# Performance work log

Measured on AMD Instinct MI355X. Metric: run time of the kernel, lower is better.

Reference implementation:

```python
import jax, jax.numpy as jnp
import numpy as np

NUM_NODES = 50000
NUM_EDGES = 1600000
NUM_GRAPHS = 64
K_HOPS = 3


def setup_inputs() -> dict:
    key = jax.random.key(0)
    ks = jax.random.split(key, 8)
    d_in, d_h, d_out = 128, 512, 16
    x = jax.random.normal(ks[0], (NUM_NODES, d_in), dtype=jnp.float32)
    edge_index = jax.random.randint(ks[1], (2, NUM_EDGES), 0, NUM_NODES, dtype=jnp.int64)
    batch = jnp.sort(jax.random.randint(ks[2], (NUM_NODES,), 0, NUM_GRAPHS, dtype=jnp.int64))
    w1 = jax.random.normal(ks[3], (d_in, d_h), dtype=jnp.float32) / np.sqrt(d_in)
    b1 = jnp.zeros((d_h,), dtype=jnp.float32)
    w2 = jax.random.normal(ks[4], (d_h, d_h), dtype=jnp.float32) / np.sqrt(d_h)
    b2 = jnp.zeros((d_h,), dtype=jnp.float32)
    wc = jax.random.normal(ks[5], (d_h, d_out), dtype=jnp.float32) / np.sqrt(d_h)
    bc = jnp.zeros((d_out,), dtype=jnp.float32)
    return {"x": x, "edge_index": edge_index, "batch": batch,
            "w1": w1, "b1": b1, "w2": w2, "b2": b2, "wc": wc, "bc": bc}


def _propagate(x, row, col, norm):
    # one hop: out[r] += x[c] * norm  (degree-normalized scatter-add)
    msg = x[col] * norm[:, None]                      # [E+N, d]
    return jax.ops.segment_sum(msg, row, num_segments=NUM_NODES)


def reference(x, edge_index, batch, w1, b1, w2, b2, wc, bc):
    # add self loops
    loops = jnp.arange(NUM_NODES, dtype=edge_index.dtype)
    row = jnp.concatenate([edge_index[0], loops])
    col = jnp.concatenate([edge_index[1], loops])
    deg = jax.ops.segment_sum(jnp.ones_like(row, dtype=jnp.float32), row,
                              num_segments=NUM_NODES)
    deg = jnp.clip(deg, 1.0)
    norm = 1.0 / deg[row]                             # [E+N]
    # K-hop propagation (eval mode: dropout / drop_node inactive)
    h = x
    for _ in range(K_HOPS):
        h = _propagate(h, row, col, norm)
    # MLP
    h = jax.nn.relu(h @ w1 + b1)
    h = h @ w2 + b2
    # global mean pool over graphs
    sums = jax.ops.segment_sum(h, batch, num_segments=NUM_GRAPHS)
    cnts = jax.ops.segment_sum(jnp.ones((h.shape[0],), dtype=h.dtype), batch,
                               num_segments=NUM_GRAPHS)
    pooled = sums / jnp.clip(cnts, 1.0)[:, None]      # [G, d_h]
    return pooled @ wc + bc                            # [G, out]
```

## Files before the change

kernel.cpp:

```cpp
#include <hip/hip_runtime.h>
#include <hip/hip_bf16.h>
#include <hip/hip_fp8.h>

#define N_NODES 50000
#define N_EDGES 1600000
#define N_GRAPHS 64
#define D_IN 128
#define D_H 512
#define D_OUT 16

#define NBUK 196
#define BUK_CAP 9216
#define P1_EDGES 8192
#define P1_BLOCKS ((N_EDGES + P1_EDGES - 1) / P1_EDGES)

typedef short bf16x8 __attribute__((ext_vector_type(8)));
typedef float f32x4 __attribute__((ext_vector_type(4)));

static __device__ __forceinline__ unsigned short f2bf(float f) {
    __hip_bfloat16 h = __float2bfloat16(f);
    return *(unsigned short*)&h;
}

static __device__ __forceinline__ float2 fp8x2_dec(unsigned short u) {
    __hip_fp8x2_e4m3 p;
    p.__x = (__hip_fp8x2_storage_t)u;
    return static_cast<float2>(p);
}

static __device__ __forceinline__ unsigned short fp8x2_enc(float a, float b) {
    __hip_fp8_e4m3 pa(a), pb(b);
    return (unsigned short)((unsigned)pa.__x | ((unsigned)pb.__x << 8));
}


__global__ __launch_bounds__(256) void partition_edges(const int* __restrict__ row,
                                                       const int* __restrict__ col,
                                                       int* __restrict__ bucket_cnt,
                                                       unsigned* __restrict__ edge_buf) {
    __shared__ unsigned recs[P1_EDGES];
    __shared__ unsigned sorted[P1_EDGES];
    __shared__ int hist4[4][NBUK];
    __shared__ int cur4[4][NBUK];
    __shared__ int gbase[NBUK];
    __shared__ int scan[256];
    int tid = threadIdx.x;
    int wave = tid >> 6;
    int e0 = blockIdx.x * P1_EDGES;
    int m = N_EDGES - e0; if (m > P1_EDGES) m = P1_EDGES;

    for (int i = tid; i < 4 * NBUK; i += 256) ((int*)hist4)[i] = 0;
    for (int i = tid; i < 4 * NBUK; i += 256) ((int*)cur4)[i] = 0;
    __syncthreads();
    for (int i = tid; i < m; i += 256) {
        int r = row[e0 + i];
        int c = col[e0 + i];
        int buk = r >> 8;
        recs[i] = ((unsigned)buk << 24) | ((unsigned)(r & 255) << 16) | (unsigned)c;
        atomicAdd(&hist4[wave][buk], 1);
    }
    __syncthreads();
    int tot = 0;
    if (tid < NBUK) tot = hist4[0][tid] + hist4[1][tid] + hist4[2][tid] + hist4[3][tid];
    scan[tid] = (tid < NBUK) ? tot : 0;
    __syncthreads();
    for (int off = 1; off < 256; off <<= 1) {
        int v = (tid >= off) ? scan[tid - off] : 0;
        __syncthreads();
        scan[tid] += v;
        __syncthreads();
    }
    if (tid < NBUK) {
        int run = (tid == 0) ? 0 : scan[tid - 1];
        gbase[tid] = (tot > 0) ? atomicAdd(&bucket_cnt[tid], tot) : 0;
#pragma unroll
        for (int w = 0; w < 4; ++w) {
            int c = hist4[w][tid];
            hist4[w][tid] = run;
            run += c;
        }
    }
    __syncthreads();
    for (int i = tid; i < m; i += 256) {
        unsigned rec = recs[i];
        int buk = rec >> 24;
        int rank = atomicAdd(&cur4[wave][buk], 1);
        sorted[hist4[wave][buk] + rank] = rec;
    }
    __syncthreads();
    for (int p = tid; p < m; p += 256) {
        unsigned rec = sorted[p];
        int buk = rec >> 24;
        edge_buf[(size_t)buk * BUK_CAP + gbase[buk] + (p - hist4[0][buk])] = rec;
    }
}

__global__ __launch_bounds__(256) void finalize_csr(const unsigned* __restrict__ edge_buf,
                                                    const int* __restrict__ bucket_cnt,
                                                    int* __restrict__ rowptr,
                                                    float* __restrict__ invdeg,
                                                    unsigned short* __restrict__ csr_col) {
    __shared__ int hist[256], excl[256], cur[256], scan[256];
    int b = blockIdx.x;
    int tid = threadIdx.x;
    scan[tid] = (tid < NBUK) ? bucket_cnt[tid] : 0;
    __syncthreads();
    for (int off = 1; off < 256; off <<= 1) {
        int v = (tid >= off) ? scan[tid - off] : 0;
        __syncthreads();
        scan[tid] += v;
        __syncthreads();
    }
    int cnt = bucket_cnt[b];
    int base = (b == 0) ? 0 : scan[b - 1];
    const unsigned* src = edge_buf + (size_t)b * BUK_CAP;
    __syncthreads();
    hist[tid] = 0; cur[tid] = 0;
    __syncthreads();
    for (int i = tid; i < cnt; i += 256)
        atomicAdd(&hist[(src[i] >> 16) & 255], 1);
    __syncthreads();
    scan[tid] = hist[tid];
    __syncthreads();
    for (int off = 1; off < 256; off <<= 1) {
        int v = (tid >= off) ? scan[tid - off] : 0;
        __syncthreads();
        scan[tid] += v;
        __syncthreads();
    }
    excl[tid] = (tid == 0) ? 0 : scan[tid - 1];
    __syncthreads();
    int r = b * 256 + tid;
    if (r < N_NODES) {
        rowptr[r] = base + excl[tid];
        invdeg[r] = 1.0f / (float)(hist[tid] + 1);
    }
    if (b == NBUK - 1 && tid == 0) rowptr[N_NODES] = base + cnt;
    for (int i = tid; i < cnt; i += 256) {
        unsigned rec = src[i];
        int rl = (rec >> 16) & 255;
        int pos = excl[rl] + atomicAdd(&cur[rl], 1);
        csr_col[base + pos] = (unsigned short)(rec & 0xFFFFu);
    }
}


__global__ __launch_bounds__(256) void convert_x(const float* __restrict__ x,
                                                 unsigned short* __restrict__ xf, int npairs) {
    int i = blockIdx.x * 256 + threadIdx.x;
    if (i < npairs) {
        float2 v = ((const float2*)x)[i];
        xf[i] = fp8x2_enc(v.x, v.y);
    }
}

__global__ __launch_bounds__(256) void make_w1p(const float* __restrict__ w1,
                                                unsigned short* __restrict__ w1p) {
    int i = blockIdx.x * 256 + threadIdx.x;
    int j = i & 7, lane = (i >> 3) & 63, s = (i >> 9) & 3, t = i >> 11;
    int k = s * 32 + (lane >> 4) * 8 + j;
    int n = t * 16 + (lane & 15);
    w1p[i] = f2bf(w1[(size_t)k * D_H + n]);
}

__global__ __launch_bounds__(256) void fold_w(const float* __restrict__ w2,
                                              const float* __restrict__ wc,
                                              const float* __restrict__ b2,
                                              const float* __restrict__ bc,
                                              const int* __restrict__ batch,
                                              float* __restrict__ wcomb,
                                              float* __restrict__ bcomb,
                                              int* __restrict__ gcnt) {
    int tid = threadIdx.x;
    if (blockIdx.x == 33) {
        if (tid < N_GRAPHS) {
            int g = tid;
            int lo = 0, hi = N_NODES;
            while (lo < hi) { int mid = (lo + hi) >> 1; if (batch[mid] < g) lo = mid + 1; else hi = mid; }
            int a = lo;
            lo = 0; hi = N_NODES;
            while (lo < hi) { int mid = (lo + hi) >> 1; if (batch[mid] < g + 1) lo = mid + 1; else hi = mid; }
            gcnt[g] = lo - a;
        }
        return;
    }
    int o = tid & 15, kl = tid >> 4;
    int k = blockIdx.x * 16 + kl;
    if (k > D_H) return;
    const float* wr = (k < D_H) ? (w2 + (size_t)k * D_H) : b2;
    float s = 0.f;
    for (int j = 0; j < D_H; j += 4) {
        s += wr[j + 0] * wc[(j + 0) * D_OUT + o]
           + wr[j + 1] * wc[(j + 1) * D_OUT + o]
           + wr[j + 2] * wc[(j + 2) * D_OUT + o]
           + wr[j + 3] * wc[(j + 3) * D_OUT + o];
    }
    if (k < D_H) wcomb[k * D_OUT + o] = s;
    else         bcomb[o] = s + bc[o];
}


__global__ __launch_bounds__(128) void propagate_fp8(const unsigned short* __restrict__ xin,
                                                     unsigned short* __restrict__ out8,
                                                     unsigned* __restrict__ out16,
                                                     int last, float extra,
                                                     const int* __restrict__ rowptr,
                                                     const unsigned short* __restrict__ csr_col,
                                                     const float* __restrict__ invdeg) {
    int wave = threadIdx.x >> 6;
    int lane = threadIdx.x & 63;
    int r = blockIdx.x * 2 + wave;
    if (r >= N_NODES) return;
    int beg = rowptr[r], end = rowptr[r + 1];
    float2 sv = fp8x2_dec(xin[(size_t)r * 64 + lane]);
    float acc0 = sv.x, acc1 = sv.y;
    for (int cs = beg; cs < end; cs += 64) {
        int nn = end - cs; if (nn > 64) nn = 64;
        int colv = (int)csr_col[cs + (lane < nn ? lane : 0)];
        int j = 0;
        for (; j + 16 <= nn; j += 16) {
            unsigned short uu[16];
#pragma unroll
            for (int q = 0; q < 16; ++q) {
                int c = __shfl(colv, j + q, 64);
                uu[q] = xin[(size_t)c * 64 + lane];
            }
#pragma unroll
            for (int q = 0; q < 16; ++q) {
                float2 v = fp8x2_dec(uu[q]);
                acc0 += v.x; acc1 += v.y;
            }
        }
        for (; j + 4 <= nn; j += 4) {
            unsigned short u0, u1, u2, u3;
            {
                int c0 = __shfl(colv, j + 0, 64), c1 = __shfl(colv, j + 1, 64);
                int c2 = __shfl(colv, j + 2, 64), c3 = __shfl(colv, j + 3, 64);
                u0 = xin[(size_t)c0 * 64 + lane];
                u1 = xin[(size_t)c1 * 64 + lane];
                u2 = xin[(size_t)c2 * 64 + lane];
                u3 = xin[(size_t)c3 * 64 + lane];
            }
            float2 v0 = fp8x2_dec(u0), v1 = fp8x2_dec(u1);
            float2 v2 = fp8x2_dec(u2), v3 = fp8x2_dec(u3);
            acc0 += v0.x + v1.x + v2.x + v3.x;
            acc1 += v0.y + v1.y + v2.y + v3.y;
        }
        for (; j < nn; ++j) {
            int c = __shfl(colv, j, 64);
            float2 v = fp8x2_dec(xin[(size_t)c * 64 + lane]);
            acc0 += v.x; acc1 += v.y;
        }
    }
    float s = invdeg[r] * extra;
    acc0 *= s; acc1 *= s;
    if (last) {
        out16[(size_t)r * 64 + lane] = (unsigned)f2bf(acc0) | ((unsigned)f2bf(acc1) << 16);
    } else {
        out8[(size_t)r * 64 + lane] = fp8x2_enc(acc0, acc1);
    }
}


__global__ __launch_bounds__(256) void gemm_mfma_pool(const unsigned short* __restrict__ h3b,
                                                      const unsigned short* __restrict__ w1p,
                                                      const float* __restrict__ b1,
                                                      const int* __restrict__ batch,
                                                      float* __restrict__ gsum) {
    __shared__ float hls[64][132];
    __shared__ int bls[64];
    int tid = threadIdx.x;
    int lane = tid & 63, wave = tid >> 6;
    int quad = lane >> 4, l15 = lane & 15;
    int mbase = blockIdx.x * 64;
    int nbase = blockIdx.y * 128;

    int m = mbase + wave * 16 + l15;
    int mc = m < N_NODES ? m : N_NODES - 1;
    const unsigned short* arow = h3b + (size_t)mc * 128 + quad * 8;
    bf16x8 afrag[4];
#pragma unroll
    for (int s = 0; s < 4; ++s)
        afrag[s] = *(const bf16x8*)(arow + s * 32);

    f32x4 acc[8];
#pragma unroll
    for (int t = 0; t < 8; ++t) acc[t] = (f32x4){0.f, 0.f, 0.f, 0.f};

    const unsigned short* bbase = w1p + ((size_t)(blockIdx.y * 8) * 4 * 64 + lane) * 8;
#pragma unroll
    for (int t = 0; t < 8; ++t) {
#pragma unroll
        for (int s = 0; s < 4; ++s) {
            bf16x8 bfrag = *(const bf16x8*)(bbase + (size_t)(t * 4 + s) * 64 * 8);
            acc[t] = __builtin_amdgcn_mfma_f32_16x16x32_bf16(afrag[s], bfrag, acc[t], 0, 0, 0);
        }
    }

    if (tid < 64) {
        int mm = mbase + tid;
        bls[tid] = (mm < N_NODES) ? batch[mm] : 0;
    }
#pragma unroll
    for (int t = 0; t < 8; ++t)
#pragma unroll
        for (int rg = 0; rg < 4; ++rg)
            hls[wave * 16 + quad * 4 + rg][t * 16 + l15] = acc[t][rg];
    __syncthreads();

    int c = tid & 127, half = tid >> 7;
    float bias = b1[nbase + c];
    int r0 = half * 32;
    int cur = bls[r0];
    float s = 0.f;
    for (int r = r0; r < r0 + 32; ++r) {
        int mm = mbase + r;
        if (mm >= N_NODES) break;
        int g = bls[r];
        float v = hls[r][c] + bias;
        v = v > 0.f ? v : 0.f;
        if (g != cur) { atomicAdd(&gsum[cur * D_H + nbase + c], s); s = 0.f; cur = g; }
        s += v;
    }
    atomicAdd(&gsum[cur * D_H + nbase + c], s);
}


__global__ __launch_bounds__(256) void final_pool(const float* __restrict__ gsum,
                                                  const int* __restrict__ gcnt,
                                                  const float* __restrict__ wcomb,
                                                  const float* __restrict__ bcomb,
                                                  float* __restrict__ out) {
    int g = blockIdx.x;
    int tid = threadIdx.x;
    __shared__ float p[D_H];
    __shared__ float part[16][17];
    int c = gcnt[g]; if (c < 1) c = 1;
    float inv = 1.0f / (float)c;
    p[tid] = gsum[g * D_H + tid] * inv;
    p[tid + 256] = gsum[g * D_H + tid + 256] * inv;
    __syncthreads();
    int o = tid & 15, ch = tid >> 4;
    int k0 = ch * 32;
    float s = 0.f;
    for (int k = k0; k < k0 + 32; ++k)
        s += p[k] * wcomb[k * D_OUT + o];
    part[ch][o] = s;
    __syncthreads();
    if (tid < D_OUT) {
        float t = bcomb[tid];
        for (int ch2 = 0; ch2 < 16; ++ch2) t += part[ch2][tid];
        out[g * D_OUT + tid] = t;
    }
}


extern "C" void kernel_launch(void* const* d_in, const int* in_sizes, int n_in,
                              void* d_out, int out_size, void* d_ws, size_t ws_size,
                              hipStream_t stream) {
    const float* x     = (const float*)d_in[0];
    const int*   eidx  = (const int*)d_in[1];
    const int*   batch = (const int*)d_in[2];
    const float* w1    = (const float*)d_in[3];
    const float* b1    = (const float*)d_in[4];
    const float* w2    = (const float*)d_in[5];
    const float* b2    = (const float*)d_in[6];
    const float* wc    = (const float*)d_in[7];
    const float* bc    = (const float*)d_in[8];
    float* out = (float*)d_out;
    const int* row = eidx;
    const int* col = eidx + N_EDGES;

    char* p = (char*)d_ws;
    auto alloc = [&](size_t bytes) { char* q = p; p += (bytes + 255) & ~(size_t)255; return q; };
    char* zbase = p;
    int*   bucket_cnt = (int*)alloc((size_t)NBUK * 4);
    float* gsum       = (float*)alloc((size_t)N_GRAPHS * D_H * 4);
    size_t zbytes = (size_t)(p - zbase);
    int*   rowptr  = (int*)alloc((size_t)(N_NODES + 1) * 4);
    int*   gcnt    = (int*)alloc((size_t)N_GRAPHS * 4);
    float* invdeg  = (float*)alloc((size_t)N_NODES * 4);
    float* wcomb   = (float*)alloc((size_t)D_H * D_OUT * 4);
    float* bcomb   = (float*)alloc((size_t)D_OUT * 4);
    unsigned* edge_buf = (unsigned*)alloc((size_t)NBUK * BUK_CAP * 4);
    unsigned short* csr_col = (unsigned short*)alloc((size_t)N_EDGES * 2);
    unsigned short* xf  = (unsigned short*)alloc((size_t)N_NODES * 64 * 2);
    unsigned short* h0f = (unsigned short*)alloc((size_t)N_NODES * 64 * 2);
    unsigned short* h1f = (unsigned short*)alloc((size_t)N_NODES * 64 * 2);
    unsigned* h3b  = (unsigned*)alloc((size_t)N_NODES * 64 * 4);
    unsigned short* w1p = (unsigned short*)alloc((size_t)D_IN * D_H * 2);

    (void)hipMemsetAsync(zbase, 0, zbytes, stream);

    convert_x<<<(N_NODES * 64 + 255) / 256, 256, 0, stream>>>(x, xf, N_NODES * 64);
    make_w1p<<<(D_IN * D_H) / 256, 256, 0, stream>>>(w1, w1p);
    fold_w<<<34, 256, 0, stream>>>(w2, wc, b2, bc, batch, wcomb, bcomb, gcnt);

    partition_edges<<<P1_BLOCKS, 256, 0, stream>>>(row, col, bucket_cnt, edge_buf);
    finalize_csr<<<NBUK, 256, 0, stream>>>(edge_buf, bucket_cnt, rowptr, invdeg, csr_col);

    int pgrid = (N_NODES + 1) / 2;
    propagate_fp8<<<pgrid, 128, 0, stream>>>(xf,  h0f, nullptr, 0, 8.0f,
                                             rowptr, csr_col, invdeg);
    propagate_fp8<<<pgrid, 128, 0, stream>>>(h0f, h1f, nullptr, 0, 8.0f,
                                             rowptr, csr_col, invdeg);
    propagate_fp8<<<pgrid, 128, 0, stream>>>(h1f, nullptr, h3b, 1, 1.0f / 64.0f,
                                             rowptr, csr_col, invdeg);

    dim3 ggrid((N_NODES + 63) / 64, D_H / 128);
    gemm_mfma_pool<<<ggrid, 256, 0, stream>>>((const unsigned short*)h3b, w1p, b1, batch, gsum);
    final_pool<<<N_GRAPHS, 256, 0, stream>>>(gsum, gcnt, wcomb, bcomb, out);
}
```

Baseline: 287.9 us.

## Use finer CSR buckets with larger blocks and fuse prep kernels

Halves the row-bucket width from 256 to 128 rows, which doubles the bucket count and halves the per-block edge chunk, and runs partition and finalize with 512 threads. The goal is more CSR-build parallelism: more finalize blocks and less shared memory per partition block. Separately, the x-to-fp8 conversion, the w1 repack and the weight folding are merged into one launch to cut launch overhead. The trade-off is longer scans and more global bucket atomics per block, and the buffer capacity of 4608 leaves less slack for skewed buckets.

```diff
diff --git a/kernel.cpp b/kernel.cpp
--- a/kernel.cpp
+++ b/kernel.cpp
@@ -9,9 +9,9 @@
 #define D_H 512
 #define D_OUT 16
 
-#define NBUK 196
-#define BUK_CAP 9216
-#define P1_EDGES 8192
+#define NBUK 391
+#define BUK_CAP 4608
+#define P1_EDGES 4096
 #define P1_BLOCKS ((N_EDGES + P1_EDGES - 1) / P1_EDGES)
 
 typedef short bf16x8 __attribute__((ext_vector_type(8)));
@@ -34,7 +34,7 @@
 }
 
 
-__global__ __launch_bounds__(256) void partition_edges(const int* __restrict__ row,
+__global__ __launch_bounds__(512) void partition_edges(const int* __restrict__ row,
                                                        const int* __restrict__ col,
                                                        int* __restrict__ bucket_cnt,
                                                        unsigned* __restrict__ edge_buf) {
@@ -43,28 +43,28 @@
     __shared__ int hist4[4][NBUK];
     __shared__ int cur4[4][NBUK];
     __shared__ int gbase[NBUK];
-    __shared__ int scan[256];
+    __shared__ int scan[512];
     int tid = threadIdx.x;
-    int wave = tid >> 6;
+    int w2 = tid >> 7;
     int e0 = blockIdx.x * P1_EDGES;
     int m = N_EDGES - e0; if (m > P1_EDGES) m = P1_EDGES;
 
-    for (int i = tid; i < 4 * NBUK; i += 256) ((int*)hist4)[i] = 0;
-    for (int i = tid; i < 4 * NBUK; i += 256) ((int*)cur4)[i] = 0;
-    __syncthreads();
-    for (int i = tid; i < m; i += 256) {
+    for (int i = tid; i < 4 * NBUK; i += 512) ((int*)hist4)[i] = 0;
+    for (int i = tid; i < 4 * NBUK; i += 512) ((int*)cur4)[i] = 0;
+    __syncthreads();
+    for (int i = tid; i < m; i += 512) {
         int r = row[e0 + i];
         int c = col[e0 + i];
-        int buk = r >> 8;
-        recs[i] = ((unsigned)buk << 24) | ((unsigned)(r & 255) << 16) | (unsigned)c;
-        atomicAdd(&hist4[wave][buk], 1);
+        int buk = r >> 7;
+        recs[i] = ((unsigned)buk << 23) | ((unsigned)(r & 127) << 16) | (unsigned)c;
+        atomicAdd(&hist4[w2][buk], 1);
     }
     __syncthreads();
     int tot = 0;
     if (tid < NBUK) tot = hist4[0][tid] + hist4[1][tid] + hist4[2][tid] + hist4[3][tid];
     scan[tid] = (tid < NBUK) ? tot : 0;
     __syncthreads();
-    for (int off = 1; off < 256; off <<= 1) {
+    for (int off = 1; off < 512; off <<= 1) {
         int v = (tid >= off) ? scan[tid - off] : 0;
         __syncthreads();
         scan[tid] += v;
@@ -81,31 +81,32 @@
         }
     }
     __syncthreads();
-    for (int i = tid; i < m; i += 256) {
+    for (int i = tid; i < m; i += 512) {
         unsigned rec = recs[i];
-        int buk = rec >> 24;
-        int rank = atomicAdd(&cur4[wave][buk], 1);
-        sorted[hist4[wave][buk] + rank] = rec;
-    }
-    __syncthreads();
-    for (int p = tid; p < m; p += 256) {
+        int buk = rec >> 23;
+        int rank = atomicAdd(&cur4[w2][buk], 1);
+        sorted[hist4[w2][buk] + rank] = rec;
+    }
+    __syncthreads();
+    for (int p = tid; p < m; p += 512) {
         unsigned rec = sorted[p];
-        int buk = rec >> 24;
+        int buk = rec >> 23;
         edge_buf[(size_t)buk * BUK_CAP + gbase[buk] + (p - hist4[0][buk])] = rec;
     }
 }
 
-__global__ __launch_bounds__(256) void finalize_csr(const unsigned* __restrict__ edge_buf,
+__global__ __launch_bounds__(512) void finalize_csr(const unsigned* __restrict__ edge_buf,
                                                     const int* __restrict__ bucket_cnt,
                                                     int* __restrict__ rowptr,
                                                     float* __restrict__ invdeg,
                                                     unsigned short* __restrict__ csr_col) {
-    __shared__ int hist[256], excl[256], cur[256], scan[256];
+    __shared__ int hist[128], excl[128], cur[128];
+    __shared__ int scan[512];
     int b = blockIdx.x;
     int tid = threadIdx.x;
     scan[tid] = (tid < NBUK) ? bucket_cnt[tid] : 0;
     __syncthreads();
-    for (int off = 1; off < 256; off <<= 1) {
+    for (int off = 1; off < 512; off <<= 1) {
         int v = (tid >= off) ? scan[tid - off] : 0;
         __syncthreads();
         scan[tid] += v;
@@ -115,64 +116,66 @@
     int base = (b == 0) ? 0 : scan[b - 1];
     const unsigned* src = edge_buf + (size_t)b * BUK_CAP;
     __syncthreads();
-    hist[tid] = 0; cur[tid] = 0;
-    __syncthreads();
-    for (int i = tid; i < cnt; i += 256)
-        atomicAdd(&hist[(src[i] >> 16) & 255], 1);
-    __syncthreads();
-    scan[tid] = hist[tid];
-    __syncthreads();
-    for (int off = 1; off < 256; off <<= 1) {
+    if (tid < 128) { hist[tid] = 0; cur[tid] = 0; }
+    __syncthreads();
+    for (int i = tid; i < cnt; i += 512)
+        atomicAdd(&hist[(src[i] >> 16) & 127], 1);
+    __syncthreads();
+    scan[tid] = (tid < 128) ? hist[tid] : 0;
+    __syncthreads();
+    for (int off = 1; off < 512; off <<= 1) {
         int v = (tid >= off) ? scan[tid - off] : 0;
         __syncthreads();
         scan[tid] += v;
         __syncthreads();
     }
-    excl[tid] = (tid == 0) ? 0 : scan[tid - 1];
-    __syncthreads();
-    int r = b * 256 + tid;
-    if (r < N_NODES) {
+    if (tid < 128) excl[tid] = (tid == 0) ? 0 : scan[tid - 1];
+    __syncthreads();
+    int r = b * 128 + tid;
+    if (tid < 128 && r < N_NODES) {
         rowptr[r] = base + excl[tid];
         invdeg[r] = 1.0f / (float)(hist[tid] + 1);
     }
     if (b == NBUK - 1 && tid == 0) rowptr[N_NODES] = base + cnt;
-    for (int i = tid; i < cnt; i += 256) {
+    for (int i = tid; i < cnt; i += 512) {
         unsigned rec = src[i];
-        int rl = (rec >> 16) & 255;
+        int rl = (rec >> 16) & 127;
         int pos = excl[rl] + atomicAdd(&cur[rl], 1);
         csr_col[base + pos] = (unsigned short)(rec & 0xFFFFu);
     }
 }
 
 
-__global__ __launch_bounds__(256) void convert_x(const float* __restrict__ x,
-                                                 unsigned short* __restrict__ xf, int npairs) {
-    int i = blockIdx.x * 256 + threadIdx.x;
-    if (i < npairs) {
+__global__ __launch_bounds__(256) void prep(const float* __restrict__ x,
+                                            unsigned short* __restrict__ xf,
+                                            const float* __restrict__ w1,
+                                            unsigned short* __restrict__ w1p,
+                                            const float* __restrict__ w2,
+                                            const float* __restrict__ wc,
+                                            const float* __restrict__ b2,
+                                            const float* __restrict__ bc,
+                                            const int* __restrict__ batch,
+                                            float* __restrict__ wcomb,
+                                            float* __restrict__ bcomb,
+                                            int* __restrict__ gcnt) {
+    int b = blockIdx.x;
+    int tid = threadIdx.x;
+    if (b < 12500) {
+        int i = b * 256 + tid;
         float2 v = ((const float2*)x)[i];
         xf[i] = fp8x2_enc(v.x, v.y);
-    }
-}
-
-__global__ __launch_bounds__(256) void make_w1p(const float* __restrict__ w1,
-                                                unsigned short* __restrict__ w1p) {
-    int i = blockIdx.x * 256 + threadIdx.x;
-    int j = i & 7, lane = (i >> 3) & 63, s = (i >> 9) & 3, t = i >> 11;
-    int k = s * 32 + (lane >> 4) * 8 + j;
-    int n = t * 16 + (lane & 15);
-    w1p[i] = f2bf(w1[(size_t)k * D_H + n]);
-}
-
-__global__ __launch_bounds__(256) void fold_w(const float* __restrict__ w2,
-                                              const float* __restrict__ wc,
-                                              const float* __restrict__ b2,
-                                              const float* __restrict__ bc,
-                                              const int* __restrict__ batch,
-                                              float* __restrict__ wcomb,
-                                              float* __restrict__ bcomb,
-                                              int* __restrict__ gcnt) {
-    int tid = threadIdx.x;
-    if (blockIdx.x == 33) {
+        return;
+    }
+    if (b < 12756) {
+        int i = (b - 12500) * 256 + tid;
+        int j = i & 7, lane = (i >> 3) & 63, s = (i >> 9) & 3, t = i >> 11;
+        int k = s * 32 + (lane >> 4) * 8 + j;
+        int n = t * 16 + (lane & 15);
+        w1p[i] = f2bf(w1[(size_t)k * D_H + n]);
+        return;
+    }
+    int fb = b - 12756;
+    if (fb == 33) {
         if (tid < N_GRAPHS) {
             int g = tid;
             int lo = 0, hi = N_NODES;
@@ -185,7 +188,7 @@
         return;
     }
     int o = tid & 15, kl = tid >> 4;
-    int k = blockIdx.x * 16 + kl;
+    int k = fb * 16 + kl;
     if (k > D_H) return;
     const float* wr = (k < D_H) ? (w2 + (size_t)k * D_H) : b2;
     float s = 0.f;
@@ -392,12 +395,11 @@
 
     (void)hipMemsetAsync(zbase, 0, zbytes, stream);
 
-    convert_x<<<(N_NODES * 64 + 255) / 256, 256, 0, stream>>>(x, xf, N_NODES * 64);
-    make_w1p<<<(D_IN * D_H) / 256, 256, 0, stream>>>(w1, w1p);
-    fold_w<<<34, 256, 0, stream>>>(w2, wc, b2, bc, batch, wcomb, bcomb, gcnt);
-
-    partition_edges<<<P1_BLOCKS, 256, 0, stream>>>(row, col, bucket_cnt, edge_buf);
-    finalize_csr<<<NBUK, 256, 0, stream>>>(edge_buf, bucket_cnt, rowptr, invdeg, csr_col);
+    prep<<<12790, 256, 0, stream>>>(x, xf, w1, w1p, w2, wc, b2, bc, batch,
+                                    wcomb, bcomb, gcnt);
+
+    partition_edges<<<P1_BLOCKS, 512, 0, stream>>>(row, col, bucket_cnt, edge_buf);
+    finalize_csr<<<NBUK, 512, 0, stream>>>(edge_buf, bucket_cnt, rowptr, invdeg, csr_col);
 
     int pgrid = (N_NODES + 1) / 2;
     propagate_fp8<<<pgrid, 128, 0, stream>>>(xf,  h0f, nullptr, 0, 8.0f,
```

Result: faster. 266.8 us (-7.3%).
